# Performance work log

Hardware: AMD Instinct MI355X
Metric: run time of the kernel (lower is better)

Reference implementation:

```python
import jax, jax.numpy as jnp
import numpy as np

HW_SCALE = 64.0
B = 1048576  # batch of image pairs


def _forward_once(img, W_conv, W_linear):
    # img: (8, 8). Extract TL, TR, BL, BR 4x4 patches, each flattened to 16.
    # reshape->transpose gives quadrants in row-major order: TL, TR, BL, BR.
    patches = img.reshape(2, 4, 2, 4).transpose(0, 2, 1, 3).reshape(4, 16)
    acc1 = jax.nn.relu(patches @ W_conv)  # (4, 4)
    conv_out = jnp.clip(acc1 / HW_SCALE, -128.0, 127.0)
    # The original scalar double-loop writes conv_out row-major into row 0 of a
    # (4,16) zero matrix; rows 1-3 are zero, so the second matmul reduces to:
    acc2 = conv_out.reshape(16) @ W_linear  # (4,)
    return jnp.clip(acc2 / HW_SCALE, -128.0, 127.0)


def setup_inputs() -> dict:
    key = jax.random.key(0)
    k1, k2, k3, k4 = jax.random.split(key, 4)
    img1 = jax.random.normal(k1, (B, 8, 8), dtype=jnp.float32)
    img2 = jax.random.normal(k2, (B, 8, 8), dtype=jnp.float32)
    W_conv = jax.random.normal(k3, (16, 4), dtype=jnp.float32) * 0.1
    W_linear = jax.random.normal(k4, (16, 4), dtype=jnp.float32) * 0.1
    return {"img1": img1, "img2": img2, "W_conv": W_conv, "W_linear": W_linear}


def reference(img1, img2, W_conv, W_linear):
    f = jax.vmap(_forward_once, in_axes=(0, None, None))
    return f(img1, W_conv, W_linear), f(img2, W_conv, W_linear)
```

## Files before the change

### kernel.cpp

```cpp
#include <hip/hip_runtime.h>


__global__ __launch_bounds__(256, 4) void surrogate_kernel(
    const float* __restrict__ img1, const float* __restrict__ img2,
    const float* __restrict__ Wc,
    const float* __restrict__ Wl,
    float* __restrict__ out,
    int B)
{
    const int lane = threadIdx.x & 63;
    const int p    = lane & 3;
    const int mloc = lane >> 2;

    const float4* wc4 = (const float4*)Wc;
    const float4* wl4 = (const float4*)Wl;

    const float4 wl0 = wl4[p * 4 + 0];
    const float4 wl1 = wl4[p * 4 + 1];
    const float4 wl2 = wl4[p * 4 + 2];
    const float4 wl3 = wl4[p * 4 + 3];

    const int wavesPerBlock = blockDim.x >> 6;
    const int waveId = (int)blockIdx.x * wavesPerBlock + ((int)threadIdx.x >> 6);
    const int nWaves = (int)gridDim.x * wavesPerBlock;
    const int total  = 2 * B;
    const int cb     = (p & 1) + ((p >> 1) << 3);

    for (int g0 = waveId << 4; g0 < total; g0 += nWaves << 4) {
        const int g = g0 + mloc;
        const float4* s4 = (g0 < B)
            ? ((const float4*)img1 + ((size_t)g << 4))
            : ((const float4*)img2 + ((size_t)(g - B) << 4));

        float4 v[4];
        v[0] = s4[cb + 0];
        v[1] = s4[cb + 2];
        v[2] = s4[cb + 4];
        v[3] = s4[cb + 6];

        float4 a = make_float4(0.f, 0.f, 0.f, 0.f);
#pragma unroll
        for (int j = 0; j < 4; ++j) {
            const float4 vv = v[j];
            const float4 w0 = wc4[4 * j + 0];
            const float4 w1 = wc4[4 * j + 1];
            const float4 w2 = wc4[4 * j + 2];
            const float4 w3 = wc4[4 * j + 3];
            a.x = fmaf(vv.x, w0.x, a.x); a.y = fmaf(vv.x, w0.y, a.y);
            a.z = fmaf(vv.x, w0.z, a.z); a.w = fmaf(vv.x, w0.w, a.w);
            a.x = fmaf(vv.y, w1.x, a.x); a.y = fmaf(vv.y, w1.y, a.y);
            a.z = fmaf(vv.y, w1.z, a.z); a.w = fmaf(vv.y, w1.w, a.w);
            a.x = fmaf(vv.z, w2.x, a.x); a.y = fmaf(vv.z, w2.y, a.y);
            a.z = fmaf(vv.z, w2.z, a.z); a.w = fmaf(vv.z, w2.w, a.w);
            a.x = fmaf(vv.w, w3.x, a.x); a.y = fmaf(vv.w, w3.y, a.y);
            a.z = fmaf(vv.w, w3.z, a.z); a.w = fmaf(vv.w, w3.w, a.w);
        }

        float4 co;
        co.x = fminf(fmaxf(fmaxf(a.x, 0.f) * 0.015625f, -128.f), 127.f);
        co.y = fminf(fmaxf(fmaxf(a.y, 0.f) * 0.015625f, -128.f), 127.f);
        co.z = fminf(fmaxf(fmaxf(a.z, 0.f) * 0.015625f, -128.f), 127.f);
        co.w = fminf(fmaxf(fmaxf(a.w, 0.f) * 0.015625f, -128.f), 127.f);

        float4 t;
        t.x = fmaf(co.x, wl0.x, fmaf(co.y, wl1.x, fmaf(co.z, wl2.x, co.w * wl3.x)));
        t.y = fmaf(co.x, wl0.y, fmaf(co.y, wl1.y, fmaf(co.z, wl2.y, co.w * wl3.y)));
        t.z = fmaf(co.x, wl0.z, fmaf(co.y, wl1.z, fmaf(co.z, wl2.z, co.w * wl3.z)));
        t.w = fmaf(co.x, wl0.w, fmaf(co.y, wl1.w, fmaf(co.z, wl2.w, co.w * wl3.w)));

        t.x += __shfl_xor(t.x, 1); t.y += __shfl_xor(t.y, 1);
        t.z += __shfl_xor(t.z, 1); t.w += __shfl_xor(t.w, 1);
        t.x += __shfl_xor(t.x, 2); t.y += __shfl_xor(t.y, 2);
        t.z += __shfl_xor(t.z, 2); t.w += __shfl_xor(t.w, 2);

        if (p == 0) {
            float4 o;
            o.x = fminf(fmaxf(t.x * 0.015625f, -128.f), 127.f);
            o.y = fminf(fmaxf(t.y * 0.015625f, -128.f), 127.f);
            o.z = fminf(fmaxf(t.z * 0.015625f, -128.f), 127.f);
            o.w = fminf(fmaxf(t.w * 0.015625f, -128.f), 127.f);
            ((float4*)out)[g] = o;
        }
    }
}

extern "C" void kernel_launch(void* const* d_in, const int* in_sizes, int n_in,
                              void* d_out, int out_size, void* d_ws, size_t ws_size,
                              hipStream_t stream) {
    const float* img1 = (const float*)d_in[0];
    const float* img2 = (const float*)d_in[1];
    const float* Wc   = (const float*)d_in[2];
    const float* Wl   = (const float*)d_in[3];
    float* out = (float*)d_out;

    const int B = in_sizes[0] / 64;
    int blocks = (2 * B + 63) / 64;
    if (blocks > 2048) blocks = 2048;
    hipLaunchKernelGGL(surrogate_kernel, dim3(blocks), dim3(256), 0, stream,
                       img1, img2, Wc, Wl, out, B);
}
```

Before: 520.0 us.

## Use contiguous per-wave chunks, 2x unroll loads, and nontemporal loads/stores

```diff
diff --git a/kernel.cpp b/kernel.cpp
--- a/kernel.cpp
+++ b/kernel.cpp
@@ -1,5 +1,58 @@
 #include <hip/hip_runtime.h>
 
+
+typedef float fx4 __attribute__((ext_vector_type(4)));
+
+static __device__ __forceinline__ fx4 ntload4(const fx4* __restrict__ p) {
+    return __builtin_nontemporal_load(p);
+}
+
+static __device__ __forceinline__ fx4 forward_quad(
+    fx4 v0, fx4 v1, fx4 v2, fx4 v3,
+    const float4* __restrict__ wc4,
+    float4 wl0, float4 wl1, float4 wl2, float4 wl3)
+{
+    const fx4 vv[4] = {v0, v1, v2, v3};
+    float ax = 0.f, ay = 0.f, az = 0.f, aw = 0.f;
+#pragma unroll
+    for (int j = 0; j < 4; ++j) {
+        const fx4 v = vv[j];
+        const float4 w0 = wc4[4 * j + 0];
+        const float4 w1 = wc4[4 * j + 1];
+        const float4 w2 = wc4[4 * j + 2];
+        const float4 w3 = wc4[4 * j + 3];
+        ax = fmaf(v.x, w0.x, ax); ay = fmaf(v.x, w0.y, ay);
+        az = fmaf(v.x, w0.z, az); aw = fmaf(v.x, w0.w, aw);
+        ax = fmaf(v.y, w1.x, ax); ay = fmaf(v.y, w1.y, ay);
+        az = fmaf(v.y, w1.z, az); aw = fmaf(v.y, w1.w, aw);
+        ax = fmaf(v.z, w2.x, ax); ay = fmaf(v.z, w2.y, ay);
+        az = fmaf(v.z, w2.z, az); aw = fmaf(v.z, w2.w, aw);
+        ax = fmaf(v.w, w3.x, ax); ay = fmaf(v.w, w3.y, ay);
+        az = fmaf(v.w, w3.z, az); aw = fmaf(v.w, w3.w, aw);
+    }
+
+    const float cox = fminf(fmaxf(fmaxf(ax, 0.f) * 0.015625f, -128.f), 127.f);
+    const float coy = fminf(fmaxf(fmaxf(ay, 0.f) * 0.015625f, -128.f), 127.f);
+    const float coz = fminf(fmaxf(fmaxf(az, 0.f) * 0.015625f, -128.f), 127.f);
+    const float cow = fminf(fmaxf(fmaxf(aw, 0.f) * 0.015625f, -128.f), 127.f);
+
+    float tx = fmaf(cox, wl0.x, fmaf(coy, wl1.x, fmaf(coz, wl2.x, cow * wl3.x)));
+    float ty = fmaf(cox, wl0.y, fmaf(coy, wl1.y, fmaf(coz, wl2.y, cow * wl3.y)));
+    float tz = fmaf(cox, wl0.z, fmaf(coy, wl1.z, fmaf(coz, wl2.z, cow * wl3.z)));
+    float tw = fmaf(cox, wl0.w, fmaf(coy, wl1.w, fmaf(coz, wl2.w, cow * wl3.w)));
+
+    tx += __shfl_xor(tx, 1); ty += __shfl_xor(ty, 1);
+    tz += __shfl_xor(tz, 1); tw += __shfl_xor(tw, 1);
+    tx += __shfl_xor(tx, 2); ty += __shfl_xor(ty, 2);
+    tz += __shfl_xor(tz, 2); tw += __shfl_xor(tw, 2);
+
+    fx4 o;
+    o.x = fminf(fmaxf(tx * 0.015625f, -128.f), 127.f);
+    o.y = fminf(fmaxf(ty * 0.015625f, -128.f), 127.f);
+    o.z = fminf(fmaxf(tz * 0.015625f, -128.f), 127.f);
+    o.w = fminf(fmaxf(tw * 0.015625f, -128.f), 127.f);
+    return o;
+}
 
 __global__ __launch_bounds__(256, 4) void surrogate_kernel(
     const float* __restrict__ img1, const float* __restrict__ img2,
@@ -14,73 +67,64 @@
 
     const float4* wc4 = (const float4*)Wc;
     const float4* wl4 = (const float4*)Wl;
-
     const float4 wl0 = wl4[p * 4 + 0];
     const float4 wl1 = wl4[p * 4 + 1];
     const float4 wl2 = wl4[p * 4 + 2];
     const float4 wl3 = wl4[p * 4 + 3];
 
     const int wavesPerBlock = blockDim.x >> 6;
-    const int waveId = (int)blockIdx.x * wavesPerBlock + ((int)threadIdx.x >> 6);
-    const int nWaves = (int)gridDim.x * wavesPerBlock;
-    const int total  = 2 * B;
-    const int cb     = (p & 1) + ((p >> 1) << 3);
+    const int wid = (int)blockIdx.x * wavesPerBlock + ((int)threadIdx.x >> 6);
+    const int nW  = (int)gridDim.x * wavesPerBlock;
+    const long long total = 2LL * B;
 
-    for (int g0 = waveId << 4; g0 < total; g0 += nWaves << 4) {
-        const int g = g0 + mloc;
-        const float4* s4 = (g0 < B)
-            ? ((const float4*)img1 + ((size_t)g << 4))
-            : ((const float4*)img2 + ((size_t)(g - B) << 4));
+    long long per = (total + nW - 1) / nW;
+    per = ((per + 31) >> 5) << 5;
+    const long long start = (long long)wid * per;
+    long long end = start + per;
+    if (end > total) end = total;
 
-        float4 v[4];
-        v[0] = s4[cb + 0];
-        v[1] = s4[cb + 2];
-        v[2] = s4[cb + 4];
-        v[3] = s4[cb + 6];
+    const int cb = (p & 1) + ((p >> 1) << 3);
+    fx4* __restrict__ out4 = (fx4*)out;
 
-        float4 a = make_float4(0.f, 0.f, 0.f, 0.f);
-#pragma unroll
-        for (int j = 0; j < 4; ++j) {
-            const float4 vv = v[j];
-            const float4 w0 = wc4[4 * j + 0];
-            const float4 w1 = wc4[4 * j + 1];
-            const float4 w2 = wc4[4 * j + 2];
-            const float4 w3 = wc4[4 * j + 3];
-            a.x = fmaf(vv.x, w0.x, a.x); a.y = fmaf(vv.x, w0.y, a.y);
-            a.z = fmaf(vv.x, w0.z, a.z); a.w = fmaf(vv.x, w0.w, a.w);
-            a.x = fmaf(vv.y, w1.x, a.x); a.y = fmaf(vv.y, w1.y, a.y);
-            a.z = fmaf(vv.y, w1.z, a.z); a.w = fmaf(vv.y, w1.w, a.w);
-            a.x = fmaf(vv.z, w2.x, a.x); a.y = fmaf(vv.z, w2.y, a.y);
-            a.z = fmaf(vv.z, w2.z, a.z); a.w = fmaf(vv.z, w2.w, a.w);
-            a.x = fmaf(vv.w, w3.x, a.x); a.y = fmaf(vv.w, w3.y, a.y);
-            a.z = fmaf(vv.w, w3.z, a.z); a.w = fmaf(vv.w, w3.w, a.w);
-        }
+    long long g0 = start;
+    for (; g0 + 32 <= end; g0 += 32) {
+        const long long gA = g0 + mloc;
+        const long long gB = g0 + 16 + mloc;
+        const fx4* sA = (g0 < B)
+            ? ((const fx4*)img1 + (gA << 4))
+            : ((const fx4*)img2 + ((gA - B) << 4));
+        const fx4* sB = (g0 + 16 < B)
+            ? ((const fx4*)img1 + (gB << 4))
+            : ((const fx4*)img2 + ((gB - B) << 4));
 
-        float4 co;
-        co.x = fminf(fmaxf(fmaxf(a.x, 0.f) * 0.015625f, -128.f), 127.f);
-        co.y = fminf(fmaxf(fmaxf(a.y, 0.f) * 0.015625f, -128.f), 127.f);
-        co.z = fminf(fmaxf(fmaxf(a.z, 0.f) * 0.015625f, -128.f), 127.f);
-        co.w = fminf(fmaxf(fmaxf(a.w, 0.f) * 0.015625f, -128.f), 127.f);
+        const fx4 a0 = ntload4(sA + cb + 0);
+        const fx4 a1 = ntload4(sA + cb + 2);
+        const fx4 a2 = ntload4(sA + cb + 4);
+        const fx4 a3 = ntload4(sA + cb + 6);
+        const fx4 b0 = ntload4(sB + cb + 0);
+        const fx4 b1 = ntload4(sB + cb + 2);
+        const fx4 b2 = ntload4(sB + cb + 4);
+        const fx4 b3 = ntload4(sB + cb + 6);
 
-        float4 t;
-        t.x = fmaf(co.x, wl0.x, fmaf(co.y, wl1.x, fmaf(co.z, wl2.x, co.w * wl3.x)));
-        t.y = fmaf(co.x, wl0.y, fmaf(co.y, wl1.y, fmaf(co.z, wl2.y, co.w * wl3.y)));
-        t.z = fmaf(co.x, wl0.z, fmaf(co.y, wl1.z, fmaf(co.z, wl2.z, co.w * wl3.z)));
-        t.w = fmaf(co.x, wl0.w, fmaf(co.y, wl1.w, fmaf(co.z, wl2.w, co.w * wl3.w)));
-
-        t.x += __shfl_xor(t.x, 1); t.y += __shfl_xor(t.y, 1);
-        t.z += __shfl_xor(t.z, 1); t.w += __shfl_xor(t.w, 1);
-        t.x += __shfl_xor(t.x, 2); t.y += __shfl_xor(t.y, 2);
-        t.z += __shfl_xor(t.z, 2); t.w += __shfl_xor(t.w, 2);
+        const fx4 oA = forward_quad(a0, a1, a2, a3, wc4, wl0, wl1, wl2, wl3);
+        const fx4 oB = forward_quad(b0, b1, b2, b3, wc4, wl0, wl1, wl2, wl3);
 
         if (p == 0) {
-            float4 o;
-            o.x = fminf(fmaxf(t.x * 0.015625f, -128.f), 127.f);
-            o.y = fminf(fmaxf(t.y * 0.015625f, -128.f), 127.f);
-            o.z = fminf(fmaxf(t.z * 0.015625f, -128.f), 127.f);
-            o.w = fminf(fmaxf(t.w * 0.015625f, -128.f), 127.f);
-            ((float4*)out)[g] = o;
+            __builtin_nontemporal_store(oA, out4 + gA);
+            __builtin_nontemporal_store(oB, out4 + gB);
         }
+    }
+    if (g0 + 16 <= end) {
+        const long long gA = g0 + mloc;
+        const fx4* sA = (g0 < B)
+            ? ((const fx4*)img1 + (gA << 4))
+            : ((const fx4*)img2 + ((gA - B) << 4));
+        const fx4 a0 = ntload4(sA + cb + 0);
+        const fx4 a1 = ntload4(sA + cb + 2);
+        const fx4 a2 = ntload4(sA + cb + 4);
+        const fx4 a3 = ntload4(sA + cb + 6);
+        const fx4 oA = forward_quad(a0, a1, a2, a3, wc4, wl0, wl1, wl2, wl3);
+        if (p == 0) __builtin_nontemporal_store(oA, out4 + gA);
     }
 }
 
```

Result: slower. 585.0 us (+12.5%).
